# Kernel optimization log

Measured on AMD Instinct MI355X. Metric: run time of the kernel, lower is better.

## Reference

```python
import jax, jax.numpy as jnp
import numpy as np

L = 6          # n_layers
T = 256        # seq_len
B = 32         # batch
N = 1024       # n_features (factor_dim)
H = 16         # n_heads
HD = 64        # head_dim
PD = H * HD    # packed_dim_size == N here
FF = 4096      # dim_feedforward
EPS = 1e-5


def setup_inputs() -> dict:
    key = jax.random.key(0)
    ks = jax.random.split(key, 6)
    s = 0.02  # weight init scale (xavier-ish for these dims)
    return {
        "src": jax.random.normal(ks[0], (T, B, N), jnp.float32),
        "attn_mask": jnp.zeros((T, T), jnp.float32),  # additive mask
        "Wqkv": jax.random.normal(ks[1], (L, 3 * PD, N), jnp.float32) * s,
        "bqkv": jnp.zeros((L, 3 * PD), jnp.float32),
        "Wo": jax.random.normal(ks[2], (L, N, PD), jnp.float32) * s,
        "bo": jnp.zeros((L, N), jnp.float32),
        "ln1_g": jnp.ones((L, N), jnp.float32),
        "ln1_b": jnp.zeros((L, N), jnp.float32),
        "ln2_g": jnp.ones((L, N), jnp.float32),
        "ln2_b": jnp.zeros((L, N), jnp.float32),
        "W1": jax.random.normal(ks[3], (L, FF, N), jnp.float32) * s,
        "b1": jnp.zeros((L, FF), jnp.float32),
        "W2": jax.random.normal(ks[4], (L, N, FF), jnp.float32) * s,
        "b2": jnp.zeros((L, N), jnp.float32),
        "lnf_g": jnp.ones((N,), jnp.float32),
        "lnf_b": jnp.zeros((N,), jnp.float32),
    }


def _layer_norm(x, g, b):
    m = x.mean(-1, keepdims=True)
    v = ((x - m) ** 2).mean(-1, keepdims=True)
    return (x - m) * jax.lax.rsqrt(v + EPS) * g + b


def reference(src, attn_mask, Wqkv, bqkv, Wo, bo, ln1_g, ln1_b, ln2_g, ln2_b,
              W1, b1, W2, b2, lnf_g, lnf_b):
    inv_sqrt_hd = 1.0 / np.sqrt(HD).astype(np.float32)

    def layer(x, p):
        wqkv, bq, wo, bo_, g1, bb1n, g2, bb2n, w1, bb1, w2, bb2 = p
        # --- self-attention block (pre-norm) ---
        h = _layer_norm(x, g1, bb1n)                       # [T,B,N]
        qkv = jnp.einsum('tbn,pn->tbp', h, wqkv) + bq      # [T,B,3*PD]
        q, k, v = jnp.split(qkv, 3, axis=-1)
        q = q.reshape(T, B, H, HD) * inv_sqrt_hd
        k = k.reshape(T, B, H, HD)
        v = v.reshape(T, B, H, HD)
        scores = jnp.einsum('tbhd,sbhd->bhts', q, k) + attn_mask  # [B,H,T,T]
        probs = jax.nn.softmax(scores, axis=-1)
        o = jnp.einsum('bhts,sbhd->tbhd', probs, v).reshape(T, B, PD)
        x = x + jnp.einsum('tbp,np->tbn', o, wo) + bo_
        # --- FFN block (pre-norm) ---
        h = _layer_norm(x, g2, bb2n)
        ff = jax.nn.relu(jnp.einsum('tbn,fn->tbf', h, w1) + bb1)
        x = x + jnp.einsum('tbf,nf->tbn', ff, w2) + bb2
        return x, None

    params = (Wqkv, bqkv, Wo, bo, ln1_g, ln1_b, ln2_g, ln2_b, W1, b1, W2, b2)
    x, _ = jax.lax.scan(layer, src, params)
    return _layer_norm(x, lnf_g, lnf_b)
```

## Files before the change

kernel.cpp:

```cpp
#include <hip/hip_runtime.h>
#include <math.h>

#define TS 256
#define BS 32
#define NF 1024
#define NH 16
#define HD 64
#define PD 1024
#define FFD 4096
#define NLAYER 6
#define ROWS (TS*BS)
#define LNEPS 1e-5f

typedef unsigned int u32;
typedef __attribute__((ext_vector_type(8))) short bf16x8;
typedef __attribute__((ext_vector_type(4))) float f32x4;

__device__ __forceinline__ unsigned short f2bf(float f) {
    u32 u = __builtin_bit_cast(u32, f);
    u32 r = (u + 0x7fffu + ((u >> 16) & 1u)) >> 16;
    return (unsigned short)r;
}

__device__ __forceinline__ void async16(const void* g, void* l) {
    __builtin_amdgcn_global_load_lds(
        (const __attribute__((address_space(1))) u32*)g,
        (__attribute__((address_space(3))) u32*)l, 16, 0, 0);
}

template <int BF16OUT>
__global__ __launch_bounds__(256)
void ln_kernel(const float* __restrict__ x, void* __restrict__ y,
               const float* __restrict__ g, const float* __restrict__ b) {
    int row = blockIdx.x;
    int tid = threadIdx.x;
    const float4* xr = (const float4*)(x + (size_t)row * NF);
    float4 v = xr[tid];
    float s  = v.x + v.y + v.z + v.w;
    float ss = v.x*v.x + v.y*v.y + v.z*v.z + v.w*v.w;
    #pragma unroll
    for (int off = 32; off > 0; off >>= 1) {
        s  += __shfl_down(s,  off);
        ss += __shfl_down(ss, off);
    }
    __shared__ float ws[4], wss[4];
    int wid = tid >> 6, lane = tid & 63;
    if (lane == 0) { ws[wid] = s; wss[wid] = ss; }
    __syncthreads();
    float sum   = ws[0] + ws[1] + ws[2] + ws[3];
    float sumsq = wss[0] + wss[1] + wss[2] + wss[3];
    float mean = sum * (1.0f / NF);
    float var  = sumsq * (1.0f / NF) - mean * mean;
    float rstd = rsqrtf(var + LNEPS);
    float4 gv = ((const float4*)g)[tid];
    float4 bv = ((const float4*)b)[tid];
    float4 o;
    o.x = (v.x - mean) * rstd * gv.x + bv.x;
    o.y = (v.y - mean) * rstd * gv.y + bv.y;
    o.z = (v.z - mean) * rstd * gv.z + bv.z;
    o.w = (v.w - mean) * rstd * gv.w + bv.w;
    if (BF16OUT) {
        ushort4 ov;
        ov.x = f2bf(o.x); ov.y = f2bf(o.y); ov.z = f2bf(o.z); ov.w = f2bf(o.w);
        ((ushort4*)((unsigned short*)y + (size_t)row * NF))[tid] = ov;
    } else {
        ((float4*)((float*)y + (size_t)row * NF))[tid] = o;
    }
}

__global__ __launch_bounds__(256)
void f2bf_kernel(const float* __restrict__ in, unsigned short* __restrict__ out, int n) {
    int i = (blockIdx.x * 256 + threadIdx.x) * 4;
    if (i >= n) return;
    float4 v = *(const float4*)(in + i);
    ushort4 o;
    o.x = f2bf(v.x); o.y = f2bf(v.y); o.z = f2bf(v.z); o.w = f2bf(v.w);
    *(ushort4*)(out + i) = o;
}

template <int MODE, int RESID>
__global__ __launch_bounds__(256)
void gemm_mfma(const unsigned short* __restrict__ A, const unsigned short* __restrict__ B,
               const float* __restrict__ bias, const float* __restrict__ resid,
               void* __restrict__ Cout, int M, int N, int K) {
    __shared__ __align__(16) unsigned short sA[128 * 32];
    __shared__ __align__(16) unsigned short sB[128 * 32];
    int tid = threadIdx.x;
    int m0 = blockIdx.y * 128, n0 = blockIdx.x * 128;

    int row0 = tid >> 2;
    int c0 = (tid & 3) ^ ((row0 >> 1) & 3);
    const unsigned short* gA0 = A + (size_t)(m0 + row0) * K + c0 * 8;
    const unsigned short* gA1 = A + (size_t)(m0 + row0 + 64) * K + c0 * 8;
    const unsigned short* gB0 = B + (size_t)(n0 + row0) * K + c0 * 8;
    const unsigned short* gB1 = B + (size_t)(n0 + row0 + 64) * K + c0 * 8;
    unsigned short* lA0 = sA + tid * 8;
    unsigned short* lA1 = sA + (tid + 256) * 8;
    unsigned short* lB0 = sB + tid * 8;
    unsigned short* lB1 = sB + (tid + 256) * 8;

    int wid = tid >> 6, lane = tid & 63;
    int wm = wid >> 1, wn = wid & 1;
    int quad = lane >> 4, rl = lane & 15;

    int aoff[4], boff[4];
    #pragma unroll
    for (int t = 0; t < 4; t++) {
        int r = wm * 64 + t * 16 + rl;
        aoff[t] = r * 32 + (quad ^ ((r >> 1) & 3)) * 8;
        int rn = wn * 64 + t * 16 + rl;
        boff[t] = rn * 32 + (quad ^ ((rn >> 1) & 3)) * 8;
    }

    f32x4 acc[4][4] = {};

    for (int kt = 0; kt < K; kt += 32) {
        __syncthreads();
        async16(gA0 + kt, lA0);
        async16(gA1 + kt, lA1);
        async16(gB0 + kt, lB0);
        async16(gB1 + kt, lB1);
        __syncthreads();
        bf16x8 a[4], b[4];
        #pragma unroll
        for (int t = 0; t < 4; t++) {
            a[t] = *(const bf16x8*)(sA + aoff[t]);
            b[t] = *(const bf16x8*)(sB + boff[t]);
        }
        #pragma unroll
        for (int i = 0; i < 4; i++)
            #pragma unroll
            for (int j = 0; j < 4; j++)
                acc[i][j] = __builtin_amdgcn_mfma_f32_16x16x32_bf16(a[i], b[j], acc[i][j], 0, 0, 0);
    }

    float bvv[4];
    #pragma unroll
    for (int nt = 0; nt < 4; nt++) bvv[nt] = bias[n0 + wn * 64 + nt * 16 + rl];
    #pragma unroll
    for (int mt = 0; mt < 4; mt++) {
        #pragma unroll
        for (int nt = 0; nt < 4; nt++) {
            #pragma unroll
            for (int r = 0; r < 4; r++) {
                int row = m0 + wm * 64 + mt * 16 + quad * 4 + r;
                int col = n0 + wn * 64 + nt * 16 + rl;
                float v = acc[mt][nt][r] + bvv[nt];
                if (MODE == 0) {
                    if (RESID) v += resid[(size_t)row * N + col];
                    ((float*)Cout)[(size_t)row * N + col] = v;
                } else if (MODE == 1) {
                    v = fmaxf(v, 0.0f);
                    ((unsigned short*)Cout)[(size_t)row * N + col] = f2bf(v);
                } else {
                    int t = row >> 5, bb = row & 31;
                    int s = col >> 10, hh = (col >> 6) & 15, d = col & 63;
                    if (s == 0) v *= 0.125f;
                    ((unsigned short*)Cout)[((((size_t)s * BS + bb) * NH + hh) * TS + t) * HD + d] = f2bf(v);
                }
            }
        }
    }
}

__global__ __launch_bounds__(256, 2)
void attn_mfma(const unsigned short* __restrict__ qkvT, const float* __restrict__ mask,
               unsigned short* __restrict__ o) {
    int bx = blockIdx.x;
    int bh = bx >> 1, half = bx & 1;
    int b = bh >> 4, h = bh & 15;
    const unsigned short* qB = qkvT + (size_t)bh * TS * HD;
    const unsigned short* kB = qB + (size_t)BS * NH * TS * HD;
    const unsigned short* vB = kB + (size_t)BS * NH * TS * HD;
    int tid = threadIdx.x, lane = tid & 63, wid = tid >> 6;
    int quad = lane >> 4, rl = lane & 15;
    int tbase = half * 128 + wid * 32;

    __shared__ __align__(16) unsigned short sKV[18432];
    __shared__ __align__(16) unsigned short sP[4][1280];

    #pragma unroll
    for (int it = 0; it < 8; it++) {
        int idx = it * 256 + tid, rrow = idx >> 3, ch = idx & 7;
        *(uint4*)(sKV + rrow * 72 + ch * 8) = *(const uint4*)(kB + (size_t)rrow * 64 + ch * 8);
    }

    bf16x8 qf[2][2];
    #pragma unroll
    for (int mt = 0; mt < 2; mt++)
        #pragma unroll
        for (int ks = 0; ks < 2; ks++)
            qf[mt][ks] = *(const bf16x8*)(qB + (size_t)(tbase + mt * 16 + rl) * 64 + ks * 32 + quad * 8);

    __syncthreads();

    f32x4 S[2][16] = {};
    #pragma unroll
    for (int nt = 0; nt < 16; nt++) {
        bf16x8 k0 = *(const bf16x8*)(sKV + (nt * 16 + rl) * 72 + quad * 8);
        bf16x8 k1 = *(const bf16x8*)(sKV + (nt * 16 + rl) * 72 + 32 + quad * 8);
        #pragma unroll
        for (int mt = 0; mt < 2; mt++) {
            S[mt][nt] = __builtin_amdgcn_mfma_f32_16x16x32_bf16(qf[mt][0], k0, S[mt][nt], 0, 0, 0);
            S[mt][nt] = __builtin_amdgcn_mfma_f32_16x16x32_bf16(qf[mt][1], k1, S[mt][nt], 0, 0, 0);
        }
    }

    float linv[2][4];
    #pragma unroll
    for (int mt = 0; mt < 2; mt++) {
        #pragma unroll
        for (int r = 0; r < 4; r++) {
            int tg = tbase + mt * 16 + quad * 4 + r;
            const float* mrow = mask + (size_t)tg * TS + rl;
            float mx = -3.0e38f;
            #pragma unroll
            for (int nt = 0; nt < 16; nt++) {
                S[mt][nt][r] += mrow[nt * 16];
                mx = fmaxf(mx, S[mt][nt][r]);
            }
            mx = fmaxf(mx, __shfl_xor(mx, 1));
            mx = fmaxf(mx, __shfl_xor(mx, 2));
            mx = fmaxf(mx, __shfl_xor(mx, 4));
            mx = fmaxf(mx, __shfl_xor(mx, 8));
            float sum = 0.0f;
            #pragma unroll
            for (int nt = 0; nt < 16; nt++) {
                float p = __expf(S[mt][nt][r] - mx);
                S[mt][nt][r] = p;
                sum += p;
            }
            sum += __shfl_xor(sum, 1);
            sum += __shfl_xor(sum, 2);
            sum += __shfl_xor(sum, 4);
            sum += __shfl_xor(sum, 8);
            linv[mt][r] = 1.0f / sum;
        }
    }

    __syncthreads();
    #pragma unroll
    for (int it = 0; it < 8; it++) {
        int idx = it * 256 + tid, srow = idx >> 3, dc = idx & 7;
        bf16x8 vv = *(const bf16x8*)(vB + (size_t)srow * 64 + dc * 8);
        #pragma unroll
        for (int j = 0; j < 8; j++)
            sKV[(dc * 8 + j) * 264 + srow] = (unsigned short)vv[j];
    }
    __syncthreads();

    f32x4 O[2][4] = {};
    unsigned short* myP = sP[wid];
    #pragma unroll
    for (int sc = 0; sc < 8; sc++) {
        #pragma unroll
        for (int mt = 0; mt < 2; mt++)
            #pragma unroll
            for (int hi = 0; hi < 2; hi++)
                #pragma unroll
                for (int r = 0; r < 4; r++)
                    myP[(mt * 16 + quad * 4 + r) * 40 + hi * 16 + rl] = f2bf(S[mt][2 * sc + hi][r]);
        bf16x8 pa[2], vf[4];
        #pragma unroll
        for (int mt = 0; mt < 2; mt++)
            pa[mt] = *(const bf16x8*)(myP + (mt * 16 + rl) * 40 + quad * 8);
        #pragma unroll
        for (int nd = 0; nd < 4; nd++)
            vf[nd] = *(const bf16x8*)(sKV + (nd * 16 + rl) * 264 + sc * 32 + quad * 8);
        #pragma unroll
        for (int mt = 0; mt < 2; mt++)
            #pragma unroll
            for (int nd = 0; nd < 4; nd++)
                O[mt][nd] = __builtin_amdgcn_mfma_f32_16x16x32_bf16(pa[mt], vf[nd], O[mt][nd], 0, 0, 0);
    }

    #pragma unroll
    for (int mt = 0; mt < 2; mt++)
        #pragma unroll
        for (int nd = 0; nd < 4; nd++)
            #pragma unroll
            for (int r = 0; r < 4; r++) {
                int tg = tbase + mt * 16 + quad * 4 + r;
                int d = nd * 16 + rl;
                o[(size_t)(tg * BS + b) * PD + h * HD + d] = f2bf(O[mt][nd][r] * linv[mt][r]);
            }
}

extern "C" void kernel_launch(void* const* d_in, const int* in_sizes, int n_in,
                              void* d_out, int out_size, void* d_ws, size_t ws_size,
                              hipStream_t stream) {
    const float* src  = (const float*)d_in[0];
    const float* mask = (const float*)d_in[1];
    const float* Wqkv = (const float*)d_in[2];
    const float* bqkv = (const float*)d_in[3];
    const float* Wo   = (const float*)d_in[4];
    const float* bo   = (const float*)d_in[5];
    const float* ln1g = (const float*)d_in[6];
    const float* ln1b = (const float*)d_in[7];
    const float* ln2g = (const float*)d_in[8];
    const float* ln2b = (const float*)d_in[9];
    const float* W1   = (const float*)d_in[10];
    const float* b1   = (const float*)d_in[11];
    const float* W2   = (const float*)d_in[12];
    const float* b2   = (const float*)d_in[13];
    const float* lnfg = (const float*)d_in[14];
    const float* lnfb = (const float*)d_in[15];

    float* x = (float*)d_out;
    char* ws = (char*)d_ws;
    unsigned short* qkvT = (unsigned short*)ws;
    unsigned short* ff   = (unsigned short*)ws;
    unsigned short* h    = (unsigned short*)(ws + 100663296);
    unsigned short* o    = (unsigned short*)(ws + 117440512);
    unsigned short* wbuf = (unsigned short*)(ws + 134217728);

    hipMemcpyAsync(x, src, (size_t)ROWS * NF * 4, hipMemcpyDeviceToDevice, stream);

    for (int l = 0; l < NLAYER; l++) {
        const float* wqkv_l = Wqkv + (size_t)l * 3 * PD * NF;
        const float* bqkv_l = bqkv + (size_t)l * 3 * PD;
        const float* wo_l   = Wo + (size_t)l * NF * PD;
        const float* bo_l   = bo + (size_t)l * NF;
        const float* w1_l   = W1 + (size_t)l * FFD * NF;
        const float* b1_l   = b1 + (size_t)l * FFD;
        const float* w2_l   = W2 + (size_t)l * NF * FFD;
        const float* b2_l   = b2 + (size_t)l * NF;

        ln_kernel<1><<<ROWS, 256, 0, stream>>>(x, h, ln1g + (size_t)l * NF, ln1b + (size_t)l * NF);
        f2bf_kernel<<<3 * PD * NF / 1024, 256, 0, stream>>>(wqkv_l, wbuf, 3 * PD * NF);
        gemm_mfma<2, 0><<<dim3(3 * PD / 128, ROWS / 128), 256, 0, stream>>>(
            h, wbuf, bqkv_l, nullptr, qkvT, ROWS, 3 * PD, NF);
        attn_mfma<<<BS * NH * 2, 256, 0, stream>>>(qkvT, mask, o);
        f2bf_kernel<<<NF * PD / 1024, 256, 0, stream>>>(wo_l, wbuf, NF * PD);
        gemm_mfma<0, 1><<<dim3(NF / 128, ROWS / 128), 256, 0, stream>>>(
            o, wbuf, bo_l, x, x, ROWS, NF, PD);
        ln_kernel<1><<<ROWS, 256, 0, stream>>>(x, h, ln2g + (size_t)l * NF, ln2b + (size_t)l * NF);
        f2bf_kernel<<<FFD * NF / 1024, 256, 0, stream>>>(w1_l, wbuf, FFD * NF);
        gemm_mfma<1, 0><<<dim3(FFD / 128, ROWS / 128), 256, 0, stream>>>(
            h, wbuf, b1_l, nullptr, ff, ROWS, FFD, NF);
        f2bf_kernel<<<NF * FFD / 1024, 256, 0, stream>>>(w2_l, wbuf, NF * FFD);
        gemm_mfma<0, 1><<<dim3(NF / 128, ROWS / 128), 256, 0, stream>>>(
            ff, wbuf, b2_l, x, x, ROWS, NF, FFD);
    }
    ln_kernel<0><<<ROWS, 256, 0, stream>>>(x, x, lnfg, lnfb);
}
```

Baseline: 2.489 ms.

## Deepen GEMM K-tile to 64, add grouped block swizzle, batch weight casts

The GEMM now stages a 64-wide K slice per iteration with an 8-way XOR swizzle in LDS. That halves the number of barrier pairs per K loop at the cost of twice the shared memory per block. Block indices are remapped into groups of 8 M-tiles so concurrently running blocks share A and B tiles in L2. The four per-layer weight fp32-to-bf16 conversions are merged into one launch writing separate buffers, which cuts launch count but needs more workspace for the weight copies.

```diff
diff --git a/kernel.cpp b/kernel.cpp
--- a/kernel.cpp
+++ b/kernel.cpp
@@ -69,13 +69,24 @@
 }
 
 __global__ __launch_bounds__(256)
-void f2bf_kernel(const float* __restrict__ in, unsigned short* __restrict__ out, int n) {
+void f2bf4_kernel(const float* __restrict__ s0, const float* __restrict__ s1,
+                  const float* __restrict__ s2, const float* __restrict__ s3,
+                  unsigned short* __restrict__ d0, unsigned short* __restrict__ d1,
+                  unsigned short* __restrict__ d2, unsigned short* __restrict__ d3,
+                  int n0, int n1, int n2, int n3) {
+    const float* s; unsigned short* d; int n;
+    switch (blockIdx.y) {
+        case 0: s = s0; d = d0; n = n0; break;
+        case 1: s = s1; d = d1; n = n1; break;
+        case 2: s = s2; d = d2; n = n2; break;
+        default: s = s3; d = d3; n = n3; break;
+    }
     int i = (blockIdx.x * 256 + threadIdx.x) * 4;
     if (i >= n) return;
-    float4 v = *(const float4*)(in + i);
+    float4 v = *(const float4*)(s + i);
     ushort4 o;
     o.x = f2bf(v.x); o.y = f2bf(v.y); o.z = f2bf(v.z); o.w = f2bf(v.w);
-    *(ushort4*)(out + i) = o;
+    *(ushort4*)(d + i) = o;
 }
 
 template <int MODE, int RESID>
@@ -83,55 +94,66 @@
 void gemm_mfma(const unsigned short* __restrict__ A, const unsigned short* __restrict__ B,
                const float* __restrict__ bias, const float* __restrict__ resid,
                void* __restrict__ Cout, int M, int N, int K) {
-    __shared__ __align__(16) unsigned short sA[128 * 32];
-    __shared__ __align__(16) unsigned short sB[128 * 32];
+    __shared__ __align__(16) unsigned short sA[128 * 64];
+    __shared__ __align__(16) unsigned short sB[128 * 64];
     int tid = threadIdx.x;
-    int m0 = blockIdx.y * 128, n0 = blockIdx.x * 128;
-
-    int row0 = tid >> 2;
-    int c0 = (tid & 3) ^ ((row0 >> 1) & 3);
-    const unsigned short* gA0 = A + (size_t)(m0 + row0) * K + c0 * 8;
-    const unsigned short* gA1 = A + (size_t)(m0 + row0 + 64) * K + c0 * 8;
-    const unsigned short* gB0 = B + (size_t)(n0 + row0) * K + c0 * 8;
-    const unsigned short* gB1 = B + (size_t)(n0 + row0 + 64) * K + c0 * 8;
-    unsigned short* lA0 = sA + tid * 8;
-    unsigned short* lA1 = sA + (tid + 256) * 8;
-    unsigned short* lB0 = sB + tid * 8;
-    unsigned short* lB1 = sB + (tid + 256) * 8;
+
+    int Nb = N >> 7;
+    int bid = blockIdx.x;
+    int group = bid / (8 * Nb);
+    int rem = bid - group * (8 * Nb);
+    int m0 = (group * 8 + rem / Nb) * 128;
+    int n0 = (rem % Nb) * 128;
+
+    int rB = tid >> 3;
+    int c0 = (tid & 7) ^ (rB & 7);
+    const unsigned short* gA[4];
+    const unsigned short* gB[4];
+    #pragma unroll
+    for (int it = 0; it < 4; it++) {
+        gA[it] = A + (size_t)(m0 + rB + 32 * it) * K + c0 * 8;
+        gB[it] = B + (size_t)(n0 + rB + 32 * it) * K + c0 * 8;
+    }
 
     int wid = tid >> 6, lane = tid & 63;
     int wm = wid >> 1, wn = wid & 1;
     int quad = lane >> 4, rl = lane & 15;
 
-    int aoff[4], boff[4];
-    #pragma unroll
-    for (int t = 0; t < 4; t++) {
-        int r = wm * 64 + t * 16 + rl;
-        aoff[t] = r * 32 + (quad ^ ((r >> 1) & 3)) * 8;
-        int rn = wn * 64 + t * 16 + rl;
-        boff[t] = rn * 32 + (quad ^ ((rn >> 1) & 3)) * 8;
-    }
+    int aoff[2][4], boff[2][4];
+    #pragma unroll
+    for (int ks = 0; ks < 2; ks++)
+        #pragma unroll
+        for (int t = 0; t < 4; t++) {
+            int r = wm * 64 + t * 16 + rl;
+            aoff[ks][t] = r * 64 + ((ks * 4 + quad) ^ (r & 7)) * 8;
+            int rn = wn * 64 + t * 16 + rl;
+            boff[ks][t] = rn * 64 + ((ks * 4 + quad) ^ (rn & 7)) * 8;
+        }
 
     f32x4 acc[4][4] = {};
 
-    for (int kt = 0; kt < K; kt += 32) {
+    for (int kt = 0; kt < K; kt += 64) {
         __syncthreads();
-        async16(gA0 + kt, lA0);
-        async16(gA1 + kt, lA1);
-        async16(gB0 + kt, lB0);
-        async16(gB1 + kt, lB1);
+        #pragma unroll
+        for (int it = 0; it < 4; it++) {
+            async16(gA[it] + kt, sA + (tid + 256 * it) * 8);
+            async16(gB[it] + kt, sB + (tid + 256 * it) * 8);
+        }
         __syncthreads();
-        bf16x8 a[4], b[4];
-        #pragma unroll
-        for (int t = 0; t < 4; t++) {
-            a[t] = *(const bf16x8*)(sA + aoff[t]);
-            b[t] = *(const bf16x8*)(sB + boff[t]);
-        }
-        #pragma unroll
-        for (int i = 0; i < 4; i++)
-            #pragma unroll
-            for (int j = 0; j < 4; j++)
-                acc[i][j] = __builtin_amdgcn_mfma_f32_16x16x32_bf16(a[i], b[j], acc[i][j], 0, 0, 0);
+        #pragma unroll
+        for (int ks = 0; ks < 2; ks++) {
+            bf16x8 a[4], b[4];
+            #pragma unroll
+            for (int t = 0; t < 4; t++) {
+                a[t] = *(const bf16x8*)(sA + aoff[ks][t]);
+                b[t] = *(const bf16x8*)(sB + boff[ks][t]);
+            }
+            #pragma unroll
+            for (int i = 0; i < 4; i++)
+                #pragma unroll
+                for (int j = 0; j < 4; j++)
+                    acc[i][j] = __builtin_amdgcn_mfma_f32_16x16x32_bf16(a[i], b[j], acc[i][j], 0, 0, 0);
+        }
     }
 
     float bvv[4];
@@ -310,9 +332,13 @@
     char* ws = (char*)d_ws;
     unsigned short* qkvT = (unsigned short*)ws;
     unsigned short* ff   = (unsigned short*)ws;
-    unsigned short* h    = (unsigned short*)(ws + 100663296);
-    unsigned short* o    = (unsigned short*)(ws + 117440512);
-    unsigned short* wbuf = (unsigned short*)(ws + 134217728);
+    unsigned short* h    = (unsigned short*)(ws + 67108864);
+    unsigned short* o    = (unsigned short*)(ws + 83886080);
+    unsigned short* wbuf = (unsigned short*)(ws + 100663296);
+    unsigned short* wq = wbuf;
+    unsigned short* wo = wbuf + 3145728;
+    unsigned short* w1 = wbuf + 4194304;
+    unsigned short* w2 = wbuf + 8388608;
 
     hipMemcpyAsync(x, src, (size_t)ROWS * NF * 4, hipMemcpyDeviceToDevice, stream);
 
@@ -326,21 +352,20 @@
         const float* w2_l   = W2 + (size_t)l * NF * FFD;
         const float* b2_l   = b2 + (size_t)l * NF;
 
+        f2bf4_kernel<<<dim3(4096, 4), 256, 0, stream>>>(
+            wqkv_l, wo_l, w1_l, w2_l, wq, wo, w1, w2,
+            3 * PD * NF, NF * PD, FFD * NF, NF * FFD);
         ln_kernel<1><<<ROWS, 256, 0, stream>>>(x, h, ln1g + (size_t)l * NF, ln1b + (size_t)l * NF);
-        f2bf_kernel<<<3 * PD * NF / 1024, 256, 0, stream>>>(wqkv_l, wbuf, 3 * PD * NF);
-        gemm_mfma<2, 0><<<dim3(3 * PD / 128, ROWS / 128), 256, 0, stream>>>(
-            h, wbuf, bqkv_l, nullptr, qkvT, ROWS, 3 * PD, NF);
+        gemm_mfma<2, 0><<<(ROWS / 128) * (3 * PD / 128), 256, 0, stream>>>(
+            h, wq, bqkv_l, nullptr, qkvT, ROWS, 3 * PD, NF);
         attn_mfma<<<BS * NH * 2, 256, 0, stream>>>(qkvT, mask, o);
-        f2bf_kernel<<<NF * PD / 1024, 256, 0, stream>>>(wo_l, wbuf, NF * PD);
-        gemm_mfma<0, 1><<<dim3(NF / 128, ROWS / 128), 256, 0, stream>>>(
-            o, wbuf, bo_l, x, x, ROWS, NF, PD);
+        gemm_mfma<0, 1><<<(ROWS / 128) * (NF / 128), 256, 0, stream>>>(
+            o, wo, bo_l, x, x, ROWS, NF, PD);
         ln_kernel<1><<<ROWS, 256, 0, stream>>>(x, h, ln2g + (size_t)l * NF, ln2b + (size_t)l * NF);
-        f2bf_kernel<<<FFD * NF / 1024, 256, 0, stream>>>(w1_l, wbuf, FFD * NF);
-        gemm_mfma<1, 0><<<dim3(FFD / 128, ROWS / 128), 256, 0, stream>>>(
-            h, wbuf, b1_l, nullptr, ff, ROWS, FFD, NF);
-        f2bf_kernel<<<NF * FFD / 1024, 256, 0, stream>>>(w2_l, wbuf, NF * FFD);
-        gemm_mfma<0, 1><<<dim3(NF / 128, ROWS / 128), 256, 0, stream>>>(
-            ff, wbuf, b2_l, x, x, ROWS, NF, FFD);
+        gemm_mfma<1, 0><<<(ROWS / 128) * (FFD / 128), 256, 0, stream>>>(
+            h, w1, b1_l, nullptr, ff, ROWS, FFD, NF);
+        gemm_mfma<0, 1><<<(ROWS / 128) * (NF / 128), 256, 0, stream>>>(
+            ff, w2, b2_l, x, x, ROWS, NF, FFD);
     }
     ln_kernel<0><<<ROWS, 256, 0, stream>>>(x, x, lnfg, lnfb);
 }
```

After: 2.209 ms. 1.13x faster.
